# Kernel optimization log

Measured on AMD Instinct MI355X. Metric: run time of the kernel, lower is better.

The kernel has to match this reference:

```python
import jax, jax.numpy as jnp
import numpy as np
from jax import lax

B, D_IN, T, H, D_OUT = 64, 256, 256, 1024, 1


def setup_inputs() -> dict:
    key = jax.random.key(0)
    ks = jax.random.split(key, 16)
    k = 1.0 / np.sqrt(H)
    u = lambda kk, shape: jax.random.uniform(kk, shape, jnp.float32, -k, k)
    inp = {"x": jax.random.normal(ks[0], (B, D_IN, T), jnp.float32)}
    in_sizes = [D_IN, H, H]
    for l in range(3):
        inp[f"w_ih{l}"] = u(ks[1 + 4 * l], (4 * H, in_sizes[l]))
        inp[f"w_hh{l}"] = u(ks[2 + 4 * l], (4 * H, H))
        inp[f"b_ih{l}"] = u(ks[3 + 4 * l], (4 * H,))
        inp[f"b_hh{l}"] = u(ks[4 + 4 * l], (4 * H,))
    inp["fc_w"] = u(ks[13], (D_OUT, H))
    inp["fc_b"] = u(ks[14], (D_OUT,))
    return inp


def _lstm_layer(x, w_ih, w_hh, b_ih, b_hh):
    # x: [B, T, d_in] -> hidden sequence [B, T, H]; PyTorch gate order i,f,g,o
    b, h = x.shape[0], w_hh.shape[1]
    # precompute all input-side gate projections in one big GEMM: [B, T, 4H]
    xg = jnp.einsum('btd,gd->btg', x, w_ih) + b_ih + b_hh

    def step(carry, xg_t):
        h_prev, c_prev = carry
        gates = xg_t + h_prev @ w_hh.T  # [B, 4H]
        i, f, g, o = jnp.split(gates, 4, axis=-1)
        c = jax.nn.sigmoid(f) * c_prev + jax.nn.sigmoid(i) * jnp.tanh(g)
        h_new = jax.nn.sigmoid(o) * jnp.tanh(c)
        return (h_new, c), h_new

    init = (jnp.zeros((b, h), x.dtype), jnp.zeros((b, h), x.dtype))
    _, hs = lax.scan(step, init, jnp.swapaxes(xg, 0, 1))  # hs: [T, B, H]
    return jnp.swapaxes(hs, 0, 1)


def reference(x, w_ih0, w_hh0, b_ih0, b_hh0, w_ih1, w_hh1, b_ih1, b_hh1,
              w_ih2, w_hh2, b_ih2, b_hh2, fc_w, fc_b):
    # x.view(B, -1, x.size(1)): memory reinterpretation, i.e. reshape (NOT transpose)
    h = x.reshape(x.shape[0], -1, x.shape[1])  # [B, T, D_IN]
    h = _lstm_layer(h, w_ih0, w_hh0, b_ih0, b_hh0)
    h = _lstm_layer(h, w_ih1, w_hh1, b_ih1, b_hh1)
    h = _lstm_layer(h, w_ih2, w_hh2, b_ih2, b_hh2)
    return h[:, -1, :] @ fc_w.T + fc_b  # [B, D_OUT]
```

## Files before the change

### kernel.cpp

```cpp
#include <hip/hip_runtime.h>


#define BB 64
#define TT 256
#define DIN 256
#define HH 1024
#define G4 4096
#define TCHUNK 64
#define HFRAG (BB * HH)

typedef __attribute__((ext_vector_type(8))) short short8;
typedef __attribute__((ext_vector_type(4))) float floatx4;

__device__ __forceinline__ unsigned short bf16_rne(float f) {
  union { float f; unsigned int u; } v; v.f = f;
  unsigned int lsb = (v.u >> 16) & 1u;
  v.u += 0x7fffu + lsb;
  return (unsigned short)(v.u >> 16);
}
__device__ __forceinline__ float bf16_to_f(unsigned short b) {
  union { float f; unsigned int u; } v; v.u = ((unsigned int)b) << 16;
  return v.f;
}

__global__ __launch_bounds__(256) void bias_add(
    const float* __restrict__ a, const float* __restrict__ b,
    float* __restrict__ o) {
  int i = blockIdx.x * 256 + threadIdx.x;
  o[i] = a[i] + b[i];
}

__global__ __launch_bounds__(256) void pack_w(
    const float* __restrict__ w, unsigned short* __restrict__ bhi) {
  int idx = blockIdx.x * 256 + threadIdx.x;
  int lane = idx & 63;
  int kk = (idx >> 6) & 31;
  int nsub = idx >> 11;
  int n = lane & 15, q = lane >> 4;
  int jj = n >> 2, g = n & 3;
  int row = g * HH + nsub * 4 + jj;
  int kbase = kk * 32 + q * 8;
  const float* src = w + (size_t)row * HH + kbase;
  unsigned short h8[8];
#pragma unroll
  for (int e = 0; e < 8; ++e) h8[e] = bf16_rne(src[e]);
  *(short8*)(bhi + (size_t)idx * 8) = *(short8*)h8;
}

__global__ __launch_bounds__(256) void pack_wih0(
    const float* __restrict__ w, unsigned short* __restrict__ bh,
    unsigned short* __restrict__ bl) {
  int idx = blockIdx.x * 256 + threadIdx.x;
  int lane = idx & 63;
  int kk = (idx >> 6) & 7;
  int nsub = idx >> 9;
  int n = nsub * 16 + (lane & 15);
  int kbase = kk * 32 + (lane >> 4) * 8;
  const float* src = w + (size_t)n * DIN + kbase;
  unsigned short h8[8], l8[8];
#pragma unroll
  for (int e = 0; e < 8; ++e) {
    float f = src[e];
    unsigned short hb = bf16_rne(f);
    h8[e] = hb;
    l8[e] = bf16_rne(f - bf16_to_f(hb));
  }
  *(short8*)(bh + (size_t)idx * 8) = *(short8*)h8;
  *(short8*)(bl + (size_t)idx * 8) = *(short8*)l8;
}

__global__ __launch_bounds__(256) void pack_x(
    const float* __restrict__ x, unsigned short* __restrict__ ph,
    unsigned short* __restrict__ pl) {
  int idx = blockIdx.x * 256 + threadIdx.x;
  int lane = idx & 63;
  int kk = (idx >> 6) & 7;
  int mt = idx >> 9;
  int m2 = lane & 15, q = lane >> 4;
  int R = mt * 16 + m2;
  int t = R >> 6, b = R & 63;
  int k = kk * 32 + q * 8;
  const float* src = x + (size_t)b * (DIN * TT) + (size_t)t * DIN + k;
  unsigned short h8[8], l8[8];
#pragma unroll
  for (int e = 0; e < 8; ++e) {
    float f = src[e];
    unsigned short hb = bf16_rne(f);
    h8[e] = hb;
    l8[e] = bf16_rne(f - bf16_to_f(hb));
  }
  *(short8*)(ph + (size_t)idx * 8) = *(short8*)h8;
  *(short8*)(pl + (size_t)idx * 8) = *(short8*)l8;
}

__global__ __launch_bounds__(256) void proj_mfma(
    const unsigned short* __restrict__ PAh,
    const unsigned short* __restrict__ PAl,
    const unsigned short* __restrict__ PBh,
    const unsigned short* __restrict__ PBl,
    const float* __restrict__ bias, float* __restrict__ xg, int NKK) {
  const int tid = threadIdx.x, lane = tid & 63, w = tid >> 6;
  const int mw = w & 1, nw = w >> 1;
  const int mtB = blockIdx.y * 8 + mw * 4;
  const int nsB = blockIdx.x * 8 + nw * 4;
  const short8* A8h = (const short8*)PAh;
  const short8* A8l = (const short8*)PAl;
  const short8* B8h = (const short8*)PBh;
  const short8* B8l = (const short8*)PBl;
  floatx4 acc[4][4] = {};
  for (int kk = 0; kk < NKK; ++kk) {
    short8 ah[4], al[4], bh[4], bl[4];
#pragma unroll
    for (int i = 0; i < 4; ++i) {
      size_t s = ((size_t)(mtB + i) * NKK + kk) * 64 + lane;
      ah[i] = A8h[s];
      al[i] = A8l[s];
    }
#pragma unroll
    for (int j = 0; j < 4; ++j) {
      size_t s = ((size_t)(nsB + j) * NKK + kk) * 64 + lane;
      bh[j] = B8h[s];
      bl[j] = B8l[s];
    }
#pragma unroll
    for (int i = 0; i < 4; ++i)
#pragma unroll
      for (int j = 0; j < 4; ++j) {
        acc[i][j] = __builtin_amdgcn_mfma_f32_16x16x32_bf16(ah[i], bh[j], acc[i][j], 0, 0, 0);
        acc[i][j] = __builtin_amdgcn_mfma_f32_16x16x32_bf16(ah[i], bl[j], acc[i][j], 0, 0, 0);
        acc[i][j] = __builtin_amdgcn_mfma_f32_16x16x32_bf16(al[i], bh[j], acc[i][j], 0, 0, 0);
      }
  }
  const int col = lane & 15, rowq = lane >> 4;
#pragma unroll
  for (int j = 0; j < 4; ++j) {
    int n = (nsB + j) * 16 + col;
    float bz = bias[n];
#pragma unroll
    for (int i = 0; i < 4; ++i) {
      int mbase = (mtB + i) * 16 + rowq * 4;
#pragma unroll
      for (int r = 0; r < 4; ++r)
        xg[(size_t)(mbase + r) * G4 + n] = acc[i][j][r] + bz;
    }
  }
}

__global__ __launch_bounds__(512, 4) void lstm_step_diag7(
    unsigned short* __restrict__ H,
    const unsigned short* __restrict__ Whh_h0,
    const unsigned short* __restrict__ Whh_h1,
    const unsigned short* __restrict__ Whh_h2,
    const unsigned short* __restrict__ Wih_h1,
    const unsigned short* __restrict__ Wih_h2,
    const float* __restrict__ xg,
    const float* __restrict__ bias,
    float* __restrict__ c_all,
    float* __restrict__ hlast,
    int d) {
  const int l = blockIdx.z;
  const int t = d - l;
  if (t < 0 || t >= TT) return;
  __shared__ float gbuf[8][32][64];
  const int tid = threadIdx.x, lane = tid & 63, w = tid >> 6;
  const int nblk = blockIdx.x;
  const int mp = blockIdx.y;
  const int mt0 = mp * 2;
  const int ns0 = nblk * 4;

  const size_t rec_off = (size_t)(l * 2 + ((t + 1) & 1)) * HFRAG;
  const short8 *pah, *pbh;
  int kkB, kkE;
  if (l == 0) {
    pah = (const short8*)(H + rec_off);
    pbh = (const short8*)Whh_h0;
    kkB = w * 4;
    kkE = kkB + 4;
  } else {
    if (w < 4) {
      pah = (const short8*)(H + rec_off);
      pbh = (const short8*)((l == 1) ? Whh_h1 : Whh_h2);
      kkB = w * 8;
    } else {
      const size_t in_off = (size_t)((l - 1) * 2 + (t & 1)) * HFRAG;
      pah = (const short8*)(H + in_off);
      pbh = (const short8*)((l == 1) ? Wih_h1 : Wih_h2);
      kkB = (w - 4) * 8;
    }
    kkE = kkB + 8;
  }

  floatx4 acc[2][4] = {};
#pragma unroll 2
  for (int kk = kkB; kk < kkE; ++kk) {
    short8 ah[2], bh[4];
#pragma unroll
    for (int i = 0; i < 2; ++i) {
      size_t sa = ((size_t)(mt0 + i) * 32 + kk) * 64 + lane;
      ah[i] = pah[sa];
    }
#pragma unroll
    for (int j = 0; j < 4; ++j) {
      size_t sb = ((size_t)(ns0 + j) * 32 + kk) * 64 + lane;
      bh[j] = pbh[sb];
    }
#pragma unroll
    for (int i = 0; i < 2; ++i)
#pragma unroll
      for (int j = 0; j < 4; ++j)
        acc[i][j] = __builtin_amdgcn_mfma_f32_16x16x32_bf16(ah[i], bh[j], acc[i][j], 0, 0, 0);
  }
  {
    const int col = lane & 15, rowq = lane >> 4;
#pragma unroll
    for (int i = 0; i < 2; ++i)
#pragma unroll
      for (int j = 0; j < 4; ++j)
#pragma unroll
        for (int r = 0; r < 4; ++r)
          gbuf[w][i * 16 + rowq * 4 + r][j * 16 + col] = acc[i][j][r];
  }
  __syncthreads();
  {
    const int bl = tid >> 4;
    const int jl = tid & 15;
    const int nl0 = jl * 4;
    float4 s = *(float4*)&gbuf[0][bl][nl0];
#pragma unroll
    for (int ww = 1; ww < 8; ++ww) {
      float4 p = *(float4*)&gbuf[ww][bl][nl0];
      s.x += p.x; s.y += p.y; s.z += p.z; s.w += p.w;
    }
    const int b = mp * 32 + bl;
    const int j = nblk * 16 + jl;
    float gi, gf, gg, go;
    if (l == 0) {
      int tl = t & (TCHUNK - 1);
      const float* xgp = xg + (size_t)(tl * BB + b) * G4 + j;
      gi = s.x + xgp[0];
      gf = s.y + xgp[HH];
      gg = s.z + xgp[2 * HH];
      go = s.w + xgp[3 * HH];
    } else {
      const float* bz = bias + (size_t)l * G4;
      gi = s.x + bz[j];
      gf = s.y + bz[HH + j];
      gg = s.z + bz[2 * HH + j];
      go = s.w + bz[3 * HH + j];
    }
    size_t hidx = (size_t)b * HH + j;
    float* c_cur = c_all + (size_t)l * (BB * HH);
    float cprev = c_cur[hidx];
    float ig = 1.f / (1.f + __expf(-gi));
    float fg = 1.f / (1.f + __expf(-gf));
    float g2 = tanhf(gg);
    float og = 1.f / (1.f + __expf(-go));
    float cn = fg * cprev + ig * g2;
    float hn = og * tanhf(cn);
    c_cur[hidx] = cn;
    unsigned short hb = bf16_rne(hn);
    size_t slotN = (((size_t)(b >> 4) * 32 + (j >> 5)) * 64 +
                    ((j >> 3) & 3) * 16 + (b & 15)) * 8 + (j & 7);
    unsigned short* Nh = H + (size_t)(l * 2 + (t & 1)) * HFRAG;
    Nh[slotN] = hb;
    if (l == 2 && t == TT - 1) hlast[hidx] = hn;
  }
}

__global__ __launch_bounds__(256) void final_fc(
    const float* __restrict__ hlast, const float* __restrict__ fc_w,
    const float* __restrict__ fc_b, float* __restrict__ out) {
  int b = blockIdx.x;
  const float* hrow = hlast + (size_t)b * HH;
  float s = 0.f;
  for (int j = threadIdx.x; j < HH; j += 256) s += hrow[j] * fc_w[j];
#pragma unroll
  for (int off = 32; off > 0; off >>= 1) s += __shfl_down(s, off, 64);
  __shared__ float wsum[4];
  int wv = threadIdx.x >> 6, ln = threadIdx.x & 63;
  if (ln == 0) wsum[wv] = s;
  __syncthreads();
  if (threadIdx.x == 0) out[b] = wsum[0] + wsum[1] + wsum[2] + wsum[3] + fc_b[0];
}

extern "C" void kernel_launch(void* const* d_in, const int* in_sizes, int n_in,
                              void* d_out, int out_size, void* d_ws,
                              size_t ws_size, hipStream_t stream) {
  const float* x = (const float*)d_in[0];
  const float* w_ih[3] = {(const float*)d_in[1], (const float*)d_in[5],
                          (const float*)d_in[9]};
  const float* w_hh[3] = {(const float*)d_in[2], (const float*)d_in[6],
                          (const float*)d_in[10]};
  const float* b_ih[3] = {(const float*)d_in[3], (const float*)d_in[7],
                          (const float*)d_in[11]};
  const float* b_hh[3] = {(const float*)d_in[4], (const float*)d_in[8],
                          (const float*)d_in[12]};
  const float* fc_w = (const float*)d_in[13];
  const float* fc_b = (const float*)d_in[14];
  float* out = (float*)d_out;

  char* ws = (char*)d_ws;
  size_t off = 0;
  auto alloc = [&](size_t bytes) {
    void* p = (void*)(ws + off);
    off += (bytes + 255) & ~(size_t)255;
    return p;
  };
  unsigned short *Whh_h[3];
  for (int l = 0; l < 3; ++l)
    Whh_h[l] = (unsigned short*)alloc((size_t)G4 * HH * 2);
  unsigned short *Wih_h[3];
  for (int l = 1; l < 3; ++l)
    Wih_h[l] = (unsigned short*)alloc((size_t)G4 * HH * 2);
  unsigned short* PB0h = (unsigned short*)alloc((size_t)G4 * DIN * 2);
  unsigned short* PB0l = (unsigned short*)alloc((size_t)G4 * DIN * 2);
  float* bias_all = (float*)alloc((size_t)3 * G4 * 4);
  unsigned short* PAxh = (unsigned short*)alloc((size_t)TT * BB * DIN * 2);
  unsigned short* PAxl = (unsigned short*)alloc((size_t)TT * BB * DIN * 2);
  unsigned short* Hfr = (unsigned short*)alloc((size_t)3 * 2 * HFRAG * 2);
  float* c_all = (float*)alloc((size_t)3 * BB * HH * 4);
  float* hlast = (float*)alloc((size_t)BB * HH * 4);
  float* xg = (float*)alloc((size_t)TCHUNK * BB * G4 * 4);

  for (int l = 0; l < 3; ++l) {
    pack_w<<<2048, 256, 0, stream>>>(w_hh[l], Whh_h[l]);
    bias_add<<<16, 256, 0, stream>>>(b_ih[l], b_hh[l], bias_all + (size_t)l * G4);
  }
  pack_w<<<2048, 256, 0, stream>>>(w_ih[1], Wih_h[1]);
  pack_w<<<2048, 256, 0, stream>>>(w_ih[2], Wih_h[2]);
  pack_wih0<<<512, 256, 0, stream>>>(w_ih[0], PB0h, PB0l);
  pack_x<<<2048, 256, 0, stream>>>(x, PAxh, PAxl);

  for (int l = 0; l < 3; ++l)
    hipMemsetAsync(Hfr + (size_t)(l * 2 + 1) * HFRAG, 0,
                   (size_t)HFRAG * 2, stream);
  hipMemsetAsync(c_all, 0, (size_t)3 * BB * HH * 4, stream);

  for (int d = 0; d < TT + 2; ++d) {
    if ((d & (TCHUNK - 1)) == 0 && d < TT) {
      int c = d / TCHUNK;
      size_t aoff = (size_t)c * 256 * 8 * 512;
      proj_mfma<<<dim3(32, 32), 256, 0, stream>>>(
          PAxh + aoff, PAxl + aoff, PB0h, PB0l, bias_all, xg, 8);
    }
    lstm_step_diag7<<<dim3(64, 2, 3), 512, 0, stream>>>(
        Hfr, Whh_h[0], Whh_h[1], Whh_h[2], Wih_h[1], Wih_h[2],
        xg, bias_all, c_all, hlast, d);
  }
  final_fc<<<BB, 256, 0, stream>>>(hlast, fc_w, fc_b, out);
}
```

Baseline: 3.409 ms.

## Cover all batch rows per block to halve recurrent weight reads

The per-timestep LSTM kernel now gives each block all 64 batch rows (four M tiles) instead of 32. The grid drops from 64x2x3 to 64x3 blocks, so each slice of the recurrent and input weights is fetched once per step instead of twice. The cross-wave reduction becomes two phases: half the waves store partial sums to padded shared memory and the other half add theirs in, followed by a 4-way sum. The trade-off is fewer blocks to fill the GPU, more accumulator registers per wave (launch bound lowered to 2 blocks), and an extra barrier.

```diff
diff --git a/kernel.cpp b/kernel.cpp
--- a/kernel.cpp
+++ b/kernel.cpp
@@ -146,7 +146,7 @@
   }
 }
 
-__global__ __launch_bounds__(512, 4) void lstm_step_diag7(
+__global__ __launch_bounds__(512, 2) void lstm_step_diag8(
     unsigned short* __restrict__ H,
     const unsigned short* __restrict__ Whh_h0,
     const unsigned short* __restrict__ Whh_h1,
@@ -158,14 +158,13 @@
     float* __restrict__ c_all,
     float* __restrict__ hlast,
     int d) {
-  const int l = blockIdx.z;
+  const int l = blockIdx.y;
   const int t = d - l;
   if (t < 0 || t >= TT) return;
-  __shared__ float gbuf[8][32][64];
+  __shared__ float gbuf[4][64][68];
   const int tid = threadIdx.x, lane = tid & 63, w = tid >> 6;
+  const int s = w & 3, ph = w >> 2;
   const int nblk = blockIdx.x;
-  const int mp = blockIdx.y;
-  const int mt0 = mp * 2;
   const int ns0 = nblk * 4;
 
   const size_t rec_off = (size_t)(l * 2 + ((t + 1) & 1)) * HFRAG;
@@ -177,26 +176,24 @@
     kkB = w * 4;
     kkE = kkB + 4;
   } else {
-    if (w < 4) {
+    if (ph == 0) {
       pah = (const short8*)(H + rec_off);
       pbh = (const short8*)((l == 1) ? Whh_h1 : Whh_h2);
-      kkB = w * 8;
     } else {
       const size_t in_off = (size_t)((l - 1) * 2 + (t & 1)) * HFRAG;
       pah = (const short8*)(H + in_off);
       pbh = (const short8*)((l == 1) ? Wih_h1 : Wih_h2);
-      kkB = (w - 4) * 8;
-    }
+    }
+    kkB = s * 8;
     kkE = kkB + 8;
   }
 
-  floatx4 acc[2][4] = {};
-#pragma unroll 2
+  floatx4 acc[4][4] = {};
   for (int kk = kkB; kk < kkE; ++kk) {
-    short8 ah[2], bh[4];
-#pragma unroll
-    for (int i = 0; i < 2; ++i) {
-      size_t sa = ((size_t)(mt0 + i) * 32 + kk) * 64 + lane;
+    short8 ah[4], bh[4];
+#pragma unroll
+    for (int i = 0; i < 4; ++i) {
+      size_t sa = ((size_t)i * 32 + kk) * 64 + lane;
       ah[i] = pah[sa];
     }
 #pragma unroll
@@ -205,48 +202,61 @@
       bh[j] = pbh[sb];
     }
 #pragma unroll
-    for (int i = 0; i < 2; ++i)
+    for (int i = 0; i < 4; ++i)
 #pragma unroll
       for (int j = 0; j < 4; ++j)
         acc[i][j] = __builtin_amdgcn_mfma_f32_16x16x32_bf16(ah[i], bh[j], acc[i][j], 0, 0, 0);
   }
-  {
-    const int col = lane & 15, rowq = lane >> 4;
-#pragma unroll
-    for (int i = 0; i < 2; ++i)
+  const int col = lane & 15, rowq = lane >> 4;
+  if (ph == 0) {
+#pragma unroll
+    for (int i = 0; i < 4; ++i)
 #pragma unroll
       for (int j = 0; j < 4; ++j)
 #pragma unroll
         for (int r = 0; r < 4; ++r)
-          gbuf[w][i * 16 + rowq * 4 + r][j * 16 + col] = acc[i][j][r];
+          gbuf[s][i * 16 + rowq * 4 + r][j * 16 + col] = acc[i][j][r];
   }
   __syncthreads();
-  {
-    const int bl = tid >> 4;
-    const int jl = tid & 15;
-    const int nl0 = jl * 4;
-    float4 s = *(float4*)&gbuf[0][bl][nl0];
-#pragma unroll
-    for (int ww = 1; ww < 8; ++ww) {
-      float4 p = *(float4*)&gbuf[ww][bl][nl0];
-      s.x += p.x; s.y += p.y; s.z += p.z; s.w += p.w;
-    }
-    const int b = mp * 32 + bl;
+  if (ph == 1) {
+#pragma unroll
+    for (int i = 0; i < 4; ++i)
+#pragma unroll
+      for (int j = 0; j < 4; ++j)
+#pragma unroll
+        for (int r = 0; r < 4; ++r)
+          gbuf[s][i * 16 + rowq * 4 + r][j * 16 + col] += acc[i][j][r];
+  }
+  __syncthreads();
+  for (int o = tid; o < 1024; o += 512) {
+    const int bl = o >> 4;
+    const int jl = o & 15;
+    const int nl0 = (jl >> 2) * 16 + (jl & 3) * 4;
+    float4 s0 = *(float4*)&gbuf[0][bl][nl0];
+    float4 s1 = *(float4*)&gbuf[1][bl][nl0];
+    float4 s2 = *(float4*)&gbuf[2][bl][nl0];
+    float4 s3 = *(float4*)&gbuf[3][bl][nl0];
+    float4 sm;
+    sm.x = (s0.x + s1.x) + (s2.x + s3.x);
+    sm.y = (s0.y + s1.y) + (s2.y + s3.y);
+    sm.z = (s0.z + s1.z) + (s2.z + s3.z);
+    sm.w = (s0.w + s1.w) + (s2.w + s3.w);
+    const int b = bl;
     const int j = nblk * 16 + jl;
     float gi, gf, gg, go;
     if (l == 0) {
       int tl = t & (TCHUNK - 1);
       const float* xgp = xg + (size_t)(tl * BB + b) * G4 + j;
-      gi = s.x + xgp[0];
-      gf = s.y + xgp[HH];
-      gg = s.z + xgp[2 * HH];
-      go = s.w + xgp[3 * HH];
+      gi = sm.x + xgp[0];
+      gf = sm.y + xgp[HH];
+      gg = sm.z + xgp[2 * HH];
+      go = sm.w + xgp[3 * HH];
     } else {
       const float* bz = bias + (size_t)l * G4;
-      gi = s.x + bz[j];
-      gf = s.y + bz[HH + j];
-      gg = s.z + bz[2 * HH + j];
-      go = s.w + bz[3 * HH + j];
+      gi = sm.x + bz[j];
+      gf = sm.y + bz[HH + j];
+      gg = sm.z + bz[2 * HH + j];
+      go = sm.w + bz[3 * HH + j];
     }
     size_t hidx = (size_t)b * HH + j;
     float* c_cur = c_all + (size_t)l * (BB * HH);
@@ -343,7 +353,7 @@
       proj_mfma<<<dim3(32, 32), 256, 0, stream>>>(
           PAxh + aoff, PAxl + aoff, PB0h, PB0l, bias_all, xg, 8);
     }
-    lstm_step_diag7<<<dim3(64, 2, 3), 512, 0, stream>>>(
+    lstm_step_diag8<<<dim3(64, 3), 512, 0, stream>>>(
         Hfr, Whh_h[0], Whh_h[1], Whh_h[2], Wih_h[1], Wih_h[2],
         xg, bias_all, c_all, hlast, d);
   }
```

Result: slower. 3.749 ms (+10.0%).
